# Kernel tuning notes

Hardware: AMD Instinct MI355X
Metric: run time of the kernel (lower is better)

Reference implementation:

```python
import jax, jax.numpy as jnp
import numpy as np

# Static multi-scale spatial shapes (H, W) per level; Len_in = sum(H*W) = 17821.
SPATIAL_SHAPES = [(100, 134), (50, 67), (25, 34), (13, 17)]
NH, NL, NP = 8, 4, 4  # n_heads, n_levels, n_points


def setup_inputs() -> dict:
    key = jax.random.key(0)
    ks = iter(jax.random.split(key, 48))
    N, Lq, Dq, Dkv, Dffn = 4, 900, 256, 384, 1024
    f32 = jnp.float32
    Len_in = sum(h * w for h, w in SPATIAL_SHAPES)

    def nrm(shape, s=0.02):
        return jax.random.normal(next(ks), shape, f32) * s

    inp = dict(
        queries=jax.random.normal(next(ks), (N, Lq, Dq), f32),
        features=jax.random.normal(next(ks), (N, Len_in, Dkv), f32),
        reference_points=jax.random.uniform(next(ks), (N, Lq, NL, 2), f32),
        q_pos=jax.random.normal(next(ks), (N, Lq, Dq), f32) * 0.02,
        kv_spatial_shapes=jnp.array(SPATIAL_SHAPES, jnp.int32),
        level_start_index=jnp.array(
            np.cumsum([0] + [h * w for h, w in SPATIAL_SHAPES[:-1]]), jnp.int32),
        # self-MHA params (torch nn.MultiheadAttention layout)
        in_proj_w=nrm((3 * Dq, Dq)), in_proj_b=jnp.zeros((3 * Dq,), f32),
        mha_out_w=nrm((Dq, Dq)), mha_out_b=jnp.zeros((Dq,), f32),
        # MSDeformAttn params
        value_proj_w=nrm((Dq, Dkv)), value_proj_b=jnp.zeros((Dq,), f32),
        samp_off_w=nrm((NH * NL * NP * 2, Dq), 0.005),
        samp_off_b=nrm((NH * NL * NP * 2,), 0.1),
        attn_w_w=nrm((NH * NL * NP, Dq), 0.01),
        attn_w_b=jnp.zeros((NH * NL * NP,), f32),
        out_proj_w=nrm((Dq, Dq)), out_proj_b=jnp.zeros((Dq,), f32),
        # FFN params
        ffn_w1=nrm((Dffn, Dq)), ffn_b1=jnp.zeros((Dffn,), f32),
        ffn_w2=nrm((Dq, Dffn)), ffn_b2=jnp.zeros((Dq,), f32),
        # LayerNorms
        ln1_g=jnp.ones((Dq,), f32), ln1_b=jnp.zeros((Dq,), f32),
        ln2_g=jnp.ones((Dq,), f32), ln2_b=jnp.zeros((Dq,), f32),
        ln3_g=jnp.ones((Dq,), f32), ln3_b=jnp.zeros((Dq,), f32),
    )
    return inp


def layer_norm(x, g, b, eps=1e-5):
    m = x.mean(-1, keepdims=True)
    v = ((x - m) ** 2).mean(-1, keepdims=True)
    return (x - m) * jax.lax.rsqrt(v + eps) * g + b


def mha(q, k, v, Wqkv, bqkv, Wo, bo, nh):
    N, Lq, D = q.shape
    dh = D // nh
    Wq, Wk, Wv = jnp.split(Wqkv, 3, 0)
    bq, bk, bv = jnp.split(bqkv, 3, 0)
    qh = (q @ Wq.T + bq).reshape(N, Lq, nh, dh)
    kh = (k @ Wk.T + bk).reshape(N, -1, nh, dh)
    vh = (v @ Wv.T + bv).reshape(N, -1, nh, dh)
    scale = jnp.asarray(1.0 / np.sqrt(dh), q.dtype)
    s = jnp.einsum('bqhd,bkhd->bhqk', qh, kh) * scale
    a = jax.nn.softmax(s, -1)
    o = jnp.einsum('bhqk,bkhd->bqhd', a, vh).reshape(N, Lq, D)
    return o @ Wo.T + bo


def grid_sample_bilinear(img, grid):
    # img: (B, H, W, D); grid: (B, Lq, P, 2) in [-1, 1] (x, y)
    # torch F.grid_sample, mode='bilinear', padding_mode='zeros', align_corners=False
    B, H, W, D = img.shape
    gx = ((grid[..., 0] + 1.0) * W - 1.0) * 0.5
    gy = ((grid[..., 1] + 1.0) * H - 1.0) * 0.5
    x0 = jnp.floor(gx); y0 = jnp.floor(gy)
    x1 = x0 + 1.0; y1 = y0 + 1.0
    wx1 = gx - x0; wx0 = 1.0 - wx1
    wy1 = gy - y0; wy0 = 1.0 - wy1
    flat = img.reshape(B, H * W, D)

    def gather(xi, yi):
        valid = (xi >= 0) & (xi <= W - 1) & (yi >= 0) & (yi <= H - 1)
        xc = jnp.clip(xi, 0, W - 1).astype(jnp.int32)
        yc = jnp.clip(yi, 0, H - 1).astype(jnp.int32)
        idx = (yc * W + xc).reshape(B, -1)
        v = jnp.take_along_axis(flat, idx[..., None], axis=1)
        v = v.reshape(B, xi.shape[1], xi.shape[2], D)
        return v * valid[..., None].astype(img.dtype)

    out = (gather(x0, y0) * (wx0 * wy0)[..., None]
           + gather(x1, y0) * (wx1 * wy0)[..., None]
           + gather(x0, y1) * (wx0 * wy1)[..., None]
           + gather(x1, y1) * (wx1 * wy1)[..., None])
    return out


def decoder_layer(queries, features, reference_points, q_pos,
                  in_proj_w, in_proj_b, mha_out_w, mha_out_b,
                  value_proj_w, value_proj_b, samp_off_w, samp_off_b,
                  attn_w_w, attn_w_b, out_proj_w, out_proj_b,
                  ffn_w1, ffn_b1, ffn_w2, ffn_b2,
                  ln1_g, ln1_b, ln2_g, ln2_b, ln3_g, ln3_b):
    N, Lq, D = queries.shape
    dh = D // NH
    # --- self attention (dropout inactive: eval mode) ---
    qk = queries + q_pos
    sa = mha(qk, qk, queries, in_proj_w, in_proj_b, mha_out_w, mha_out_b, NH)
    x = layer_norm(queries + sa, ln1_g, ln1_b)
    # --- multi-scale deformable cross attention ---
    qpe = x + q_pos
    value = (features @ value_proj_w.T + value_proj_b).reshape(N, -1, NH, dh)
    off = (qpe @ samp_off_w.T + samp_off_b).reshape(N, Lq, NH, NL, NP, 2)
    aw = jax.nn.softmax(
        (qpe @ attn_w_w.T + attn_w_b).reshape(N, Lq, NH, NL * NP), -1
    ).reshape(N, Lq, NH, NL, NP)
    # offset normalizer is (W, H) per level
    normalizer = jnp.asarray([[w, h] for h, w in SPATIAL_SHAPES], x.dtype)
    loc = (reference_points[:, :, None, :, None, :]
           + off / normalizer[None, None, None, :, None, :])
    grids = 2.0 * loc - 1.0  # (N, Lq, NH, NL, NP, 2)
    out = jnp.zeros((N, Lq, NH, dh), x.dtype)
    start = 0
    for l, (h, w) in enumerate(SPATIAL_SHAPES):
        v_l = value[:, start:start + h * w]                       # (N, HW, NH, dh)
        v_l = v_l.transpose(0, 2, 1, 3).reshape(N * NH, h, w, dh)
        g_l = grids[:, :, :, l].transpose(0, 2, 1, 3, 4).reshape(N * NH, Lq, NP, 2)
        samp = grid_sample_bilinear(v_l, g_l).reshape(N, NH, Lq, NP, dh)
        w_l = aw[:, :, :, l].transpose(0, 2, 1, 3)                # (N, NH, Lq, NP)
        out = out + jnp.einsum('nhqp,nhqpd->nqhd', w_l, samp)
        start += h * w
    ca = out.reshape(N, Lq, D) @ out_proj_w.T + out_proj_b
    x = layer_norm(x + ca, ln2_g, ln2_b)
    # --- FFN ---
    f = jax.nn.relu(x @ ffn_w1.T + ffn_b1) @ ffn_w2.T + ffn_b2
    return layer_norm(x + f, ln3_g, ln3_b)


def reference(queries, features, reference_points, q_pos,
              kv_spatial_shapes, level_start_index,
              in_proj_w, in_proj_b, mha_out_w, mha_out_b,
              value_proj_w, value_proj_b, samp_off_w, samp_off_b,
              attn_w_w, attn_w_b, out_proj_w, out_proj_b,
              ffn_w1, ffn_b1, ffn_w2, ffn_b2,
              ln1_g, ln1_b, ln2_g, ln2_b, ln3_g, ln3_b):
    # kv_spatial_shapes / level_start_index mirror the torch API; the per-level
    # sizes must be static for jit, so SPATIAL_SHAPES is used internally.
    return decoder_layer(queries, features, reference_points, q_pos,
                         in_proj_w, in_proj_b, mha_out_w, mha_out_b,
                         value_proj_w, value_proj_b, samp_off_w, samp_off_b,
                         attn_w_w, attn_w_b, out_proj_w, out_proj_b,
                         ffn_w1, ffn_b1, ffn_w2, ffn_b2,
                         ln1_g, ln1_b, ln2_g, ln2_b, ln3_g, ln3_b)
```

## Files before the change

kernel.cpp:

```cpp
#include <hip/hip_runtime.h>
#include <cstddef>


typedef unsigned short u16;
typedef short  bf16x8 __attribute__((ext_vector_type(8)));
typedef float  f32x4  __attribute__((ext_vector_type(4)));

constexpr int NB=4, LQ=900, DQ=256, DKV=384, DFFN=1024, NHD=8, DH=32, LEN_IN=17821;
constexpr int MQ     = NB*LQ;
constexpr int MQ_PAD = 3648;
constexpr int MV     = NB*LEN_IN;
constexpr int MV_PAD = 557*128;
constexpr int VT_STRIDE = 912;

#define LN_EPS 1e-5f

__device__ inline u16 f2bf(float f) {
    union { float f; unsigned u; } v; v.f = f;
    unsigned u = v.u;
    u += 0x7fffu + ((u >> 16) & 1u);
    return (u16)(u >> 16);
}
__device__ inline float bf2f(u16 h) {
    union { unsigned u; float f; } v; v.u = ((unsigned)h) << 16; return v.f;
}
__device__ inline void gload_lds16(const u16* g, u16* l) {
    __builtin_amdgcn_global_load_lds(
        (const __attribute__((address_space(1))) unsigned*)g,
        (__attribute__((address_space(3))) unsigned*)l, 16, 0, 0);
}

__global__ void convert_misc_kernel(const float* __restrict__ s0, const float* __restrict__ s1,
        const float* __restrict__ s2, const float* __restrict__ s3, const float* __restrict__ s4,
        const float* __restrict__ s5, const float* __restrict__ s6, const float* __restrict__ s7,
        const float* __restrict__ s8, u16* __restrict__ dst) {
    int i4 = blockIdx.x * 256 + threadIdx.x;
    if (i4 >= 492544) return;
    size_t e = (size_t)i4 * 4;
    const float* src; size_t b;
    if      (e < 196608)  { src = s0; b = 0; }
    else if (e < 262144)  { src = s1; b = 196608; }
    else if (e < 360448)  { src = s2; b = 262144; }
    else if (e < 425984)  { src = s3; b = 360448; }
    else if (e < 458752)  { src = s4; b = 425984; }
    else if (e < 524288)  { src = s5; b = 458752; }
    else if (e < 786432)  { src = s6; b = 524288; }
    else if (e < 1048576) { src = s7; b = 786432; }
    else                  { src = s8; b = 1048576; }
    float4 v = *(const float4*)(src + (e - b));
    dst[e] = f2bf(v.x); dst[e+1] = f2bf(v.y); dst[e+2] = f2bf(v.z); dst[e+3] = f2bf(v.w);
}

__global__ void convert_features_kernel(const float* __restrict__ src, u16* __restrict__ dst) {
    size_t i8 = (size_t)blockIdx.x * 256 + threadIdx.x;
    if (i8 >= (size_t)MV * DKV / 8) return;
    const float4 a = ((const float4*)src)[i8 * 2];
    const float4 b = ((const float4*)src)[i8 * 2 + 1];
    u16 h[8] = {f2bf(a.x), f2bf(a.y), f2bf(a.z), f2bf(a.w),
                f2bf(b.x), f2bf(b.y), f2bf(b.z), f2bf(b.w)};
    *(bf16x8*)(dst + i8 * 8) = *(bf16x8*)h;
}

__global__ void addbf_kernel(const float* __restrict__ a, const float* __restrict__ b,
                             u16* __restrict__ c, int n4) {
    int i = blockIdx.x * 256 + threadIdx.x;
    if (i >= n4) return;
    float4 va = ((const float4*)a)[i];
    float4 vb = ((const float4*)b)[i];
    u16 h[4] = {f2bf(va.x + vb.x), f2bf(va.y + vb.y), f2bf(va.z + vb.z), f2bf(va.w + vb.w)};
    *(uint2*)(c + (size_t)i * 4) = *(uint2*)h;
}

template<int BM, int BN, int WM, int WN, int OMODE, bool RELU>
__global__ __launch_bounds__(256) void gemm_bf16(
        const u16* __restrict__ A, const u16* __restrict__ W,
        const float* __restrict__ bias, void* __restrict__ Cout,
        int M, int N, int K) {
    constexpr int BK = 32;
    __shared__ u16 As[BM * BK];
    __shared__ u16 Bs[BN * BK];
    const int bm = blockIdx.y * BM, bn = blockIdx.x * BN;
    const int tid = threadIdx.x, wid = tid >> 6, lane = tid & 63;
    constexpr int NWC = BN / WN;
    const int wr = wid / NWC, wc = wid % NWC;
    constexpr int MR = WM / 16, NR = WN / 16;
    f32x4 acc[MR][NR];
    #pragma unroll
    for (int i = 0; i < MR; ++i)
        #pragma unroll
        for (int j = 0; j < NR; ++j)
            acc[i][j] = (f32x4){0.f, 0.f, 0.f, 0.f};
    const int r16 = lane & 15;
    const int kb  = (lane >> 4) * 8;

    for (int k0 = 0; k0 < K; k0 += BK) {
        #pragma unroll
        for (int i = 0; i < BM / 64; ++i) {
            const int c = i * 256 + tid;
            gload_lds16(A + (size_t)(bm + (c >> 2)) * K + k0 + (c & 3) * 8, &As[c * 8]);
        }
        #pragma unroll
        for (int i = 0; i < BN / 64; ++i) {
            const int c = i * 256 + tid;
            gload_lds16(W + (size_t)(bn + (c >> 2)) * K + k0 + (c & 3) * 8, &Bs[c * 8]);
        }
        __syncthreads();
        bf16x8 af[MR], bfr[NR];
        #pragma unroll
        for (int i = 0; i < MR; ++i)
            af[i] = *(const bf16x8*)&As[(wr * WM + i * 16 + r16) * BK + kb];
        #pragma unroll
        for (int j = 0; j < NR; ++j)
            bfr[j] = *(const bf16x8*)&Bs[(wc * WN + j * 16 + r16) * BK + kb];
        #pragma unroll
        for (int i = 0; i < MR; ++i)
            #pragma unroll
            for (int j = 0; j < NR; ++j)
                acc[i][j] = __builtin_amdgcn_mfma_f32_16x16x32_bf16(af[i], bfr[j], acc[i][j], 0, 0, 0);
        __syncthreads();
    }
    float* Cf = (float*)Cout;
    u16*   Cb = (u16*)Cout;
    #pragma unroll
    for (int i = 0; i < MR; ++i) {
        #pragma unroll
        for (int j = 0; j < NR; ++j) {
            const int col   = bn + wc * WN + j * 16 + r16;
            const int rbase = bm + wr * WM + i * 16 + (lane >> 4) * 4;
            const float bv = bias[col];
            if (OMODE == 2) {
                if (rbase < M) {
                    const int nb_ = rbase / LQ, tok = rbase - nb_ * LQ;
                    u16 hv[4];
                    #pragma unroll
                    for (int r = 0; r < 4; ++r) hv[r] = f2bf(acc[i][j][r] + bv);
                    uint2 pk; pk.x = hv[0] | ((unsigned)hv[1] << 16);
                    pk.y = hv[2] | ((unsigned)hv[3] << 16);
                    *(uint2*)(Cb + ((size_t)((nb_ * NHD + (col >> 5)) * DH + (col & 31))) * VT_STRIDE + tok) = pk;
                }
            } else {
                #pragma unroll
                for (int r = 0; r < 4; ++r) {
                    const int row = rbase + r;
                    if (row < M) {
                        float v = acc[i][j][r] + bv;
                        if (RELU) v = fmaxf(v, 0.f);
                        if (OMODE == 1) Cb[(size_t)row * N + col] = f2bf(v);
                        else            Cf[(size_t)row * N + col] = v;
                    }
                }
            }
        }
    }
}

__global__ __launch_bounds__(256) void attn_mfma_kernel(
        const u16* __restrict__ qk_proj,
        const u16* __restrict__ vT,
        u16* __restrict__ attno) {
    constexpr int NT = 29;
    const int n = blockIdx.z, h = blockIdx.y;
    const int q0 = blockIdx.x * 64;
    const int tid = threadIdx.x, wid = tid >> 6;
    const int lane = tid & 63;
    const int lq = lane & 15, lg = lane >> 4;

    __shared__ u16 Kb[2][32 * 32];
    __shared__ u16 Vb[2][32 * 32];
    __shared__ u16 Pl[4][16 * 40];

    const int qg  = q0 + wid * 16 + lq;
    const int qcl = min(qg, LQ - 1);
    const bf16x8 qf = *(const bf16x8*)(qk_proj + ((size_t)(n * LQ + qcl)) * 512 + h * 32 + lg * 8);

    f32x4 acc0 = {0.f, 0.f, 0.f, 0.f};
    f32x4 acc1 = {0.f, 0.f, 0.f, 0.f};
    float m = -1e30f, l = 0.f;
    const float scale = 0.17677669529663687f;

    const int ks8 = (lg ^ ((lq >> 1) & 3)) * 8;

#define STAGE(buf, kt)                                                            \
    do {                                                                          \
        if (tid < 128) {                                                          \
            const int key = tid >> 2, sl = tid & 3;                               \
            const int slg = sl ^ ((key >> 1) & 3);                                \
            const int tok = min((kt) * 32 + key, LQ - 1);                         \
            gload_lds16(qk_proj + ((size_t)(n * LQ + tok)) * 512 + 256 + h * 32 + slg * 8, \
                        &Kb[buf][tid * 8]);                                       \
        } else {                                                                  \
            const int t2 = tid - 128;                                             \
            const int dim = t2 >> 2, sl = t2 & 3;                                 \
            const int slg = sl ^ ((dim >> 1) & 3);                                \
            gload_lds16(vT + ((size_t)((n * NHD + h) * DH + dim)) * VT_STRIDE + (kt) * 32 + slg * 8, \
                        &Vb[buf][t2 * 8]);                                        \
        }                                                                         \
    } while (0)

    STAGE(0, 0);
    __syncthreads();

    for (int kt = 0; kt < NT; ++kt) {
        const int cur = kt & 1;
        if (kt + 1 < NT) STAGE(cur ^ 1, kt + 1);

        const u16* Kc = Kb[cur];
        const u16* Vc = Vb[cur];

        const bf16x8 kf0 = *(const bf16x8*)(Kc + lq * 32 + ks8);
        const bf16x8 kf1 = *(const bf16x8*)(Kc + (16 + lq) * 32 + ks8);
        f32x4 c0 = {0.f, 0.f, 0.f, 0.f}, c1 = {0.f, 0.f, 0.f, 0.f};
        c0 = __builtin_amdgcn_mfma_f32_16x16x32_bf16(kf0, qf, c0, 0, 0, 0);
        c1 = __builtin_amdgcn_mfma_f32_16x16x32_bf16(kf1, qf, c1, 0, 0, 0);

        float s[8];
        const int kbase = kt * 32 + lg * 4;
        #pragma unroll
        for (int r = 0; r < 4; ++r) {
            s[r]     = (kbase + r      < LQ) ? c0[r] * scale : -1e30f;
            s[4 + r] = (kbase + 16 + r < LQ) ? c1[r] * scale : -1e30f;
        }
        float tmax = s[0];
        #pragma unroll
        for (int i = 1; i < 8; ++i) tmax = fmaxf(tmax, s[i]);
        tmax = fmaxf(tmax, __shfl_xor(tmax, 16));
        tmax = fmaxf(tmax, __shfl_xor(tmax, 32));
        const float mnew = fmaxf(m, tmax);
        const float corr = __expf(m - mnew);
        l *= corr;
        #pragma unroll
        for (int r = 0; r < 4; ++r) { acc0[r] *= corr; acc1[r] *= corr; }
        float p[8], ps = 0.f;
        #pragma unroll
        for (int i = 0; i < 8; ++i) { p[i] = __expf(s[i] - mnew); ps += p[i]; }
        ps += __shfl_xor(ps, 16);
        ps += __shfl_xor(ps, 32);
        l += ps;
        m = mnew;

        u16* Pw = Pl[wid];
        {
            uint2 w0, w1;
            w0.x = f2bf(p[0]) | ((unsigned)f2bf(p[1]) << 16);
            w0.y = f2bf(p[2]) | ((unsigned)f2bf(p[3]) << 16);
            w1.x = f2bf(p[4]) | ((unsigned)f2bf(p[5]) << 16);
            w1.y = f2bf(p[6]) | ((unsigned)f2bf(p[7]) << 16);
            *(uint2*)(Pw + lq * 40 + lg * 4)      = w0;
            *(uint2*)(Pw + lq * 40 + 16 + lg * 4) = w1;
        }
        asm volatile("s_waitcnt lgkmcnt(0)" ::: "memory");
        __builtin_amdgcn_sched_barrier(0);
        const bf16x8 pt = *(const bf16x8*)(Pw + lq * 40 + lg * 8);

        const bf16x8 vf0 = *(const bf16x8*)(Vc + lq * 32 + ks8);
        const bf16x8 vf1 = *(const bf16x8*)(Vc + (16 + lq) * 32 + ks8);
        acc0 = __builtin_amdgcn_mfma_f32_16x16x32_bf16(vf0, pt, acc0, 0, 0, 0);
        acc1 = __builtin_amdgcn_mfma_f32_16x16x32_bf16(vf1, pt, acc1, 0, 0, 0);

        __syncthreads();
    }
#undef STAGE

    if (qg < LQ) {
        const float inv = 1.f / l;
        u16* op = attno + ((size_t)(n * LQ + qg)) * DQ + h * DH;
        uint2 o0, o1;
        o0.x = f2bf(acc0[0] * inv) | ((unsigned)f2bf(acc0[1] * inv) << 16);
        o0.y = f2bf(acc0[2] * inv) | ((unsigned)f2bf(acc0[3] * inv) << 16);
        o1.x = f2bf(acc1[0] * inv) | ((unsigned)f2bf(acc1[1] * inv) << 16);
        o1.y = f2bf(acc1[2] * inv) | ((unsigned)f2bf(acc1[3] * inv) << 16);
        *(uint2*)(op + lg * 4)      = o0;
        *(uint2*)(op + 16 + lg * 4) = o1;
    }
}

template<bool WBF>
__global__ __launch_bounds__(64) void ln_kernel(
        const float* __restrict__ a, const float* __restrict__ b,
        const float* __restrict__ g, const float* __restrict__ beta,
        float* __restrict__ outf, u16* __restrict__ outb) {
    const int row = blockIdx.x;
    const int lane = threadIdx.x;
    const float* ap = &a[(size_t)row * DQ];
    const float* bp = &b[(size_t)row * DQ];
    float x[4];
    float s = 0.f;
    #pragma unroll
    for (int i = 0; i < 4; ++i) { x[i] = ap[lane + i * 64] + bp[lane + i * 64]; s += x[i]; }
    #pragma unroll
    for (int off = 32; off > 0; off >>= 1) s += __shfl_xor(s, off);
    const float mean = s * (1.f / DQ);
    float v = 0.f;
    #pragma unroll
    for (int i = 0; i < 4; ++i) { const float d = x[i] - mean; v += d * d; }
    #pragma unroll
    for (int off = 32; off > 0; off >>= 1) v += __shfl_xor(v, off);
    const float rstd = rsqrtf(v * (1.f / DQ) + LN_EPS);
    #pragma unroll
    for (int i = 0; i < 4; ++i) {
        const int c = lane + i * 64;
        const float y = (x[i] - mean) * rstd * g[c] + beta[c];
        outf[(size_t)row * DQ + c] = y;
        if (WBF) outb[(size_t)row * DQ + c] = f2bf(y);
    }
}

__global__ void softmax16_kernel(const float* __restrict__ in, float* __restrict__ out, int total) {
    const int i = blockIdx.x * blockDim.x + threadIdx.x;
    if (i >= total) return;
    const float* p = &in[(size_t)i * 16];
    float mx = -1e30f;
    float e[16];
    #pragma unroll
    for (int j = 0; j < 16; ++j) mx = fmaxf(mx, p[j]);
    float sum = 0.f;
    #pragma unroll
    for (int j = 0; j < 16; ++j) { e[j] = __expf(p[j] - mx); sum += e[j]; }
    const float inv = 1.f / sum;
    #pragma unroll
    for (int j = 0; j < 16; ++j) out[(size_t)i * 16 + j] = e[j] * inv;
}

__global__ __launch_bounds__(256) void deform_kernel(
        const u16* __restrict__ value,
        const float* __restrict__ ref_pts,
        const float* __restrict__ off,
        const float* __restrict__ aw,
        u16* __restrict__ out) {
    const int nq = blockIdx.x;
    const int n = nq / LQ, q = nq % LQ;
    const int h = threadIdx.x / DH, d = threadIdx.x % DH;
    const int Hs[4] = {100, 50, 25, 13};
    const int Ws[4] = {134, 67, 34, 17};
    const int LS[4] = {0, 13400, 16750, 17600};
    const float* refp = &ref_pts[((size_t)(n * LQ + q)) * 8];
    const float* offp = &off[((size_t)((n * LQ + q) * NHD + h)) * 32];
    const float* awp  = &aw[((size_t)((n * LQ + q) * NHD + h)) * 16];
    const u16* vb = &value[(size_t)n * LEN_IN * DQ + h * DH + d];
    float acc = 0.f;
    #pragma unroll
    for (int l = 0; l < 4; ++l) {
        const float Wl = (float)Ws[l], Hl = (float)Hs[l];
        const float rx = refp[l * 2 + 0], ry = refp[l * 2 + 1];
        const int Wi = Ws[l], Hi = Hs[l], base = LS[l];
        #pragma unroll
        for (int p = 0; p < 4; ++p) {
            const float ox = offp[(l * 4 + p) * 2 + 0];
            const float oy = offp[(l * 4 + p) * 2 + 1];
            const float gx = (rx + ox / Wl) * Wl - 0.5f;
            const float gy = (ry + oy / Hl) * Hl - 0.5f;
            const float x0f = floorf(gx), y0f = floorf(gy);
            const int x0 = (int)x0f, y0 = (int)y0f;
            const int x1 = x0 + 1, y1 = y0 + 1;
            const float wx1 = gx - x0f, wx0 = 1.f - wx1;
            const float wy1 = gy - y0f, wy0 = 1.f - wy1;
            float sample = 0.f;
            if (x0 >= 0 && x0 < Wi && y0 >= 0 && y0 < Hi)
                sample += wx0 * wy0 * bf2f(vb[(size_t)(base + y0 * Wi + x0) * DQ]);
            if (x1 >= 0 && x1 < Wi && y0 >= 0 && y0 < Hi)
                sample += wx1 * wy0 * bf2f(vb[(size_t)(base + y0 * Wi + x1) * DQ]);
            if (x0 >= 0 && x0 < Wi && y1 >= 0 && y1 < Hi)
                sample += wx0 * wy1 * bf2f(vb[(size_t)(base + y1 * Wi + x0) * DQ]);
            if (x1 >= 0 && x1 < Wi && y1 >= 0 && y1 < Hi)
                sample += wx1 * wy1 * bf2f(vb[(size_t)(base + y1 * Wi + x1) * DQ]);
            acc += awp[l * 4 + p] * sample;
        }
    }
    out[((size_t)(n * LQ + q)) * DQ + h * DH + d] = f2bf(acc);
}

extern "C" void kernel_launch(void* const* d_in, const int* in_sizes, int n_in,
                              void* d_out, int out_size, void* d_ws, size_t ws_size,
                              hipStream_t stream) {
    const float* queries   = (const float*)d_in[0];
    const float* features  = (const float*)d_in[1];
    const float* ref_pts   = (const float*)d_in[2];
    const float* q_pos     = (const float*)d_in[3];
    const float* in_proj_w = (const float*)d_in[6];
    const float* in_proj_b = (const float*)d_in[7];
    const float* mha_out_w = (const float*)d_in[8];
    const float* mha_out_b = (const float*)d_in[9];
    const float* value_proj_w = (const float*)d_in[10];
    const float* value_proj_b = (const float*)d_in[11];
    const float* samp_off_w = (const float*)d_in[12];
    const float* samp_off_b = (const float*)d_in[13];
    const float* attn_w_w  = (const float*)d_in[14];
    const float* attn_w_b  = (const float*)d_in[15];
    const float* out_proj_w = (const float*)d_in[16];
    const float* out_proj_b = (const float*)d_in[17];
    const float* ffn_w1    = (const float*)d_in[18];
    const float* ffn_b1    = (const float*)d_in[19];
    const float* ffn_w2    = (const float*)d_in[20];
    const float* ffn_b2    = (const float*)d_in[21];
    const float* ln1_g     = (const float*)d_in[22];
    const float* ln1_b     = (const float*)d_in[23];
    const float* ln2_g     = (const float*)d_in[24];
    const float* ln2_b     = (const float*)d_in[25];
    const float* ln3_g     = (const float*)d_in[26];
    const float* ln3_b     = (const float*)d_in[27];

    u16* u = (u16*)d_ws;
    u16* wbf      = u; u += 1982464;
    u16* qk_bf    = u; u += (size_t)MQ_PAD * 256;
    u16* qk_proj  = u; u += (size_t)MQ * 512;
    u16* vT       = u; u += (size_t)NB * NHD * DH * VT_STRIDE + 64;
    u16* attno_bf = u; u += (size_t)MQ_PAD * 256;
    u16* qpe_bf   = u; u += (size_t)MQ_PAD * 256;
    u16* x2_bf    = u; u += (size_t)MQ_PAD * 256;
    u16* dout_bf  = u; u += (size_t)MQ_PAD * 256;
    u16* ffnh_bf  = u; u += (size_t)MQ_PAD * 1024;
    u16* features_bf = u; u += (size_t)MV_PAD * DKV;
    u16* value_bf = u; u += (size_t)MV * 256;

    const u16* wIn    = wbf + 0;
    const u16* wMha   = wbf + 196608;
    const u16* wVal   = wbf + 262144;
    const u16* wSamp  = wbf + 360448;
    const u16* wAttnw = wbf + 425984;
    const u16* wOut   = wbf + 458752;
    const u16* wF1    = wbf + 524288;
    const u16* wF2    = wbf + 786432;
    const u16* queries_bf = wbf + 1048576;

    float* f = (float*)u;
    float* x1    = f; f += (size_t)MQ * 256;
    float* sa    = f; float* x2 = sa; f += (size_t)MQ * 256;
    float* offb  = f; float* ca = offb; f += (size_t)MQ * 256;
    float* awlog = f; float* ffnout = awlog; f += 460800;
    float* awbuf = f; f += 460800;

    const int n4 = MQ * 256 / 4;

    hipLaunchKernelGGL(convert_misc_kernel, dim3(1924), dim3(256), 0, stream,
                       in_proj_w, mha_out_w, value_proj_w, samp_off_w, attn_w_w,
                       out_proj_w, ffn_w1, ffn_w2, queries, wbf);
    hipLaunchKernelGGL(addbf_kernel, dim3((n4 + 255) / 256), dim3(256), 0, stream,
                       queries, q_pos, qk_bf, n4);
    hipLaunchKernelGGL((gemm_bf16<64,64,32,32,1,false>), dim3(8, 57), dim3(256), 0, stream,
                       qk_bf, wIn, in_proj_b, (void*)qk_proj, MQ, 512, 256);
    hipLaunchKernelGGL((gemm_bf16<64,64,32,32,2,false>), dim3(4, 57), dim3(256), 0, stream,
                       queries_bf, wIn + 512 * 256, in_proj_b + 512, (void*)vT, MQ, 256, 256);
    hipLaunchKernelGGL(attn_mfma_kernel, dim3(15, NHD, NB), dim3(256), 0, stream,
                       qk_proj, vT, attno_bf);
    hipLaunchKernelGGL((gemm_bf16<64,64,32,32,0,false>), dim3(4, 57), dim3(256), 0, stream,
                       attno_bf, wMha, mha_out_b, (void*)sa, MQ, 256, 256);
    hipLaunchKernelGGL((ln_kernel<false>), dim3(MQ), dim3(64), 0, stream,
                       queries, sa, ln1_g, ln1_b, x1, (u16*)nullptr);
    hipLaunchKernelGGL(addbf_kernel, dim3((n4 + 255) / 256), dim3(256), 0, stream,
                       x1, q_pos, qpe_bf, n4);
    hipLaunchKernelGGL(convert_features_kernel, dim3(13366), dim3(256), 0, stream,
                       features, features_bf);
    hipLaunchKernelGGL((gemm_bf16<128,128,64,64,1,false>), dim3(2, 557), dim3(256), 0, stream,
                       features_bf, wVal, value_proj_b, (void*)value_bf, MV, 256, DKV);
    hipLaunchKernelGGL((gemm_bf16<64,64,32,32,0,false>), dim3(4, 57), dim3(256), 0, stream,
                       qpe_bf, wSamp, samp_off_b, (void*)offb, MQ, 256, 256);
    hipLaunchKernelGGL((gemm_bf16<64,64,32,32,0,false>), dim3(2, 57), dim3(256), 0, stream,
                       qpe_bf, wAttnw, attn_w_b, (void*)awlog, MQ, 128, 256);
    hipLaunchKernelGGL(softmax16_kernel, dim3((MQ * NHD + 255) / 256), dim3(256), 0, stream,
                       awlog, awbuf, MQ * NHD);
    hipLaunchKernelGGL(deform_kernel, dim3(NB * LQ), dim3(256), 0, stream,
                       value_bf, ref_pts, offb, awbuf, dout_bf);
    hipLaunchKernelGGL((gemm_bf16<64,64,32,32,0,false>), dim3(4, 57), dim3(256), 0, stream,
                       dout_bf, wOut, out_proj_b, (void*)ca, MQ, 256, 256);
    hipLaunchKernelGGL((ln_kernel<true>), dim3(MQ), dim3(64), 0, stream,
                       x1, ca, ln2_g, ln2_b, x2, x2_bf);
    hipLaunchKernelGGL((gemm_bf16<64,64,32,32,1,true>), dim3(16, 57), dim3(256), 0, stream,
                       x2_bf, wF1, ffn_b1, (void*)ffnh_bf, MQ, DFFN, 256);
    hipLaunchKernelGGL((gemm_bf16<64,64,32,32,0,false>), dim3(4, 57), dim3(256), 0, stream,
                       ffnh_bf, wF2, ffn_b2, (void*)ffnout, MQ, 256, DFFN);
    hipLaunchKernelGGL((ln_kernel<false>), dim3(MQ), dim3(64), 0, stream,
                       x2, ffnout, ln3_g, ln3_b, (float*)d_out, (u16*)nullptr);
}
```

Baseline: 426.1 us.

## Fuse feature conversion into value GEMM, merge offset/weight GEMMs, inline softmax

Removes the separate fp32-to-bf16 features conversion pass: a new value-projection GEMM reads fp32 features directly and converts them while staging into LDS. The sampling-offset and attention-weight projections become one GEMM with N=384 and a packed bias, since their weights are adjacent in the bf16 buffer. The softmax over the attention weights now runs inside the deform kernel, and the q_pos add is folded into LayerNorm1. This cuts several launches and a large intermediate round trip through memory. The cost is that the new value GEMM issues synchronous fp32 loads without the async LDS path and uses smaller tiles, and the deform kernel recomputes the softmax in every thread.

```diff
diff --git a/kernel.cpp b/kernel.cpp
--- a/kernel.cpp
+++ b/kernel.cpp
@@ -10,7 +10,6 @@
 constexpr int MQ     = NB*LQ;
 constexpr int MQ_PAD = 3648;
 constexpr int MV     = NB*LEN_IN;
-constexpr int MV_PAD = 557*128;
 constexpr int VT_STRIDE = 912;
 
 #define LN_EPS 1e-5f
@@ -33,9 +32,19 @@
 __global__ void convert_misc_kernel(const float* __restrict__ s0, const float* __restrict__ s1,
         const float* __restrict__ s2, const float* __restrict__ s3, const float* __restrict__ s4,
         const float* __restrict__ s5, const float* __restrict__ s6, const float* __restrict__ s7,
-        const float* __restrict__ s8, u16* __restrict__ dst) {
+        const float* __restrict__ s8, u16* __restrict__ dst,
+        const float* __restrict__ sampb, const float* __restrict__ attnb,
+        float* __restrict__ pbias) {
     int i4 = blockIdx.x * 256 + threadIdx.x;
-    if (i4 >= 492544) return;
+    if (i4 >= 492544) {
+        const int e2 = (i4 - 492544) * 4;
+        if (e2 < 384) {
+            float4 v = (e2 < 256) ? *(const float4*)(sampb + e2)
+                                  : *(const float4*)(attnb + (e2 - 256));
+            *(float4*)(pbias + e2) = v;
+        }
+        return;
+    }
     size_t e = (size_t)i4 * 4;
     const float* src; size_t b;
     if      (e < 196608)  { src = s0; b = 0; }
@@ -49,16 +58,6 @@
     else                  { src = s8; b = 1048576; }
     float4 v = *(const float4*)(src + (e - b));
     dst[e] = f2bf(v.x); dst[e+1] = f2bf(v.y); dst[e+2] = f2bf(v.z); dst[e+3] = f2bf(v.w);
-}
-
-__global__ void convert_features_kernel(const float* __restrict__ src, u16* __restrict__ dst) {
-    size_t i8 = (size_t)blockIdx.x * 256 + threadIdx.x;
-    if (i8 >= (size_t)MV * DKV / 8) return;
-    const float4 a = ((const float4*)src)[i8 * 2];
-    const float4 b = ((const float4*)src)[i8 * 2 + 1];
-    u16 h[8] = {f2bf(a.x), f2bf(a.y), f2bf(a.z), f2bf(a.w),
-                f2bf(b.x), f2bf(b.y), f2bf(b.z), f2bf(b.w)};
-    *(bf16x8*)(dst + i8 * 8) = *(bf16x8*)h;
 }
 
 __global__ void addbf_kernel(const float* __restrict__ a, const float* __restrict__ b,
@@ -154,6 +153,71 @@
     }
 }
 
+__global__ __launch_bounds__(256) void gemm_value_kernel(
+        const float* __restrict__ A, const u16* __restrict__ W,
+        const float* __restrict__ bias, u16* __restrict__ C, int M) {
+    constexpr int BK = 32, BM = 64, K = DKV;
+    __shared__ u16 As[BM * BK];
+    __shared__ u16 Bs[256 * BK];
+    const int bm = blockIdx.x * BM;
+    const int tid = threadIdx.x, wid = tid >> 6, lane = tid & 63;
+    const int r16 = lane & 15, kb = (lane >> 4) * 8;
+    f32x4 acc[4][4];
+    #pragma unroll
+    for (int i = 0; i < 4; ++i)
+        #pragma unroll
+        for (int j = 0; j < 4; ++j)
+            acc[i][j] = (f32x4){0.f, 0.f, 0.f, 0.f};
+
+    const int arow = tid >> 2, ac8 = (tid & 3) * 8;
+    for (int k0 = 0; k0 < K; k0 += BK) {
+        #pragma unroll
+        for (int i = 0; i < 4; ++i) {
+            const int c = i * 256 + tid;
+            gload_lds16(W + (size_t)(c >> 2) * K + k0 + (c & 3) * 8, &Bs[c * 8]);
+        }
+        {
+            float tmp[8] = {0.f, 0.f, 0.f, 0.f, 0.f, 0.f, 0.f, 0.f};
+            if (bm + arow < M) {
+                *(float4*)tmp       = *(const float4*)(A + (size_t)(bm + arow) * K + k0 + ac8);
+                *(float4*)(tmp + 4) = *(const float4*)(A + (size_t)(bm + arow) * K + k0 + ac8 + 4);
+            }
+            u16 h8[8];
+            #pragma unroll
+            for (int j = 0; j < 8; ++j) h8[j] = f2bf(tmp[j]);
+            *(bf16x8*)&As[arow * 32 + ac8] = *(bf16x8*)h8;
+        }
+        __syncthreads();
+        bf16x8 af[4], bfr[4];
+        #pragma unroll
+        for (int i = 0; i < 4; ++i)
+            af[i] = *(const bf16x8*)&As[(i * 16 + r16) * 32 + kb];
+        #pragma unroll
+        for (int j = 0; j < 4; ++j)
+            bfr[j] = *(const bf16x8*)&Bs[(wid * 64 + j * 16 + r16) * 32 + kb];
+        #pragma unroll
+        for (int i = 0; i < 4; ++i)
+            #pragma unroll
+            for (int j = 0; j < 4; ++j)
+                acc[i][j] = __builtin_amdgcn_mfma_f32_16x16x32_bf16(af[i], bfr[j], acc[i][j], 0, 0, 0);
+        __syncthreads();
+    }
+    #pragma unroll
+    for (int i = 0; i < 4; ++i) {
+        #pragma unroll
+        for (int j = 0; j < 4; ++j) {
+            const int col   = wid * 64 + j * 16 + r16;
+            const int rbase = bm + i * 16 + (lane >> 4) * 4;
+            const float bv = bias[col];
+            #pragma unroll
+            for (int r = 0; r < 4; ++r) {
+                const int row = rbase + r;
+                if (row < M) C[(size_t)row * 256 + col] = f2bf(acc[i][j][r] + bv);
+            }
+        }
+    }
+}
+
 __global__ __launch_bounds__(256) void attn_mfma_kernel(
         const u16* __restrict__ qk_proj,
         const u16* __restrict__ vT,
@@ -274,11 +338,12 @@
     }
 }
 
-template<bool WBF>
+template<int MODE>
 __global__ __launch_bounds__(64) void ln_kernel(
         const float* __restrict__ a, const float* __restrict__ b,
         const float* __restrict__ g, const float* __restrict__ beta,
-        float* __restrict__ outf, u16* __restrict__ outb) {
+        float* __restrict__ outf, u16* __restrict__ outb,
+        const float* __restrict__ pos) {
     const int row = blockIdx.x;
     const int lane = threadIdx.x;
     const float* ap = &a[(size_t)row * DQ];
@@ -301,31 +366,15 @@
         const int c = lane + i * 64;
         const float y = (x[i] - mean) * rstd * g[c] + beta[c];
         outf[(size_t)row * DQ + c] = y;
-        if (WBF) outb[(size_t)row * DQ + c] = f2bf(y);
-    }
-}
-
-__global__ void softmax16_kernel(const float* __restrict__ in, float* __restrict__ out, int total) {
-    const int i = blockIdx.x * blockDim.x + threadIdx.x;
-    if (i >= total) return;
-    const float* p = &in[(size_t)i * 16];
-    float mx = -1e30f;
-    float e[16];
-    #pragma unroll
-    for (int j = 0; j < 16; ++j) mx = fmaxf(mx, p[j]);
-    float sum = 0.f;
-    #pragma unroll
-    for (int j = 0; j < 16; ++j) { e[j] = __expf(p[j] - mx); sum += e[j]; }
-    const float inv = 1.f / sum;
-    #pragma unroll
-    for (int j = 0; j < 16; ++j) out[(size_t)i * 16 + j] = e[j] * inv;
+        if (MODE == 1) outb[(size_t)row * DQ + c] = f2bf(y);
+        if (MODE == 2) outb[(size_t)row * DQ + c] = f2bf(y + pos[(size_t)row * DQ + c]);
+    }
 }
 
 __global__ __launch_bounds__(256) void deform_kernel(
         const u16* __restrict__ value,
         const float* __restrict__ ref_pts,
-        const float* __restrict__ off,
-        const float* __restrict__ aw,
+        const float* __restrict__ packed,
         u16* __restrict__ out) {
     const int nq = blockIdx.x;
     const int n = nq / LQ, q = nq % LQ;
@@ -334,8 +383,17 @@
     const int Ws[4] = {134, 67, 34, 17};
     const int LS[4] = {0, 13400, 16750, 17600};
     const float* refp = &ref_pts[((size_t)(n * LQ + q)) * 8];
-    const float* offp = &off[((size_t)((n * LQ + q) * NHD + h)) * 32];
-    const float* awp  = &aw[((size_t)((n * LQ + q) * NHD + h)) * 16];
+    const float* rowp = packed + (size_t)nq * 384;
+    const float* offp = rowp + h * 32;
+    const float* lgp  = rowp + 256 + h * 16;
+    float w[16];
+    float mx = lgp[0];
+    #pragma unroll
+    for (int j = 1; j < 16; ++j) mx = fmaxf(mx, lgp[j]);
+    float sum = 0.f;
+    #pragma unroll
+    for (int j = 0; j < 16; ++j) { w[j] = __expf(lgp[j] - mx); sum += w[j]; }
+    const float winv = 1.f / sum;
     const u16* vb = &value[(size_t)n * LEN_IN * DQ + h * DH + d];
     float acc = 0.f;
     #pragma unroll
@@ -363,10 +421,10 @@
                 sample += wx0 * wy1 * bf2f(vb[(size_t)(base + y1 * Wi + x0) * DQ]);
             if (x1 >= 0 && x1 < Wi && y1 >= 0 && y1 < Hi)
                 sample += wx1 * wy1 * bf2f(vb[(size_t)(base + y1 * Wi + x1) * DQ]);
-            acc += awp[l * 4 + p] * sample;
-        }
-    }
-    out[((size_t)(n * LQ + q)) * DQ + h * DH + d] = f2bf(acc);
+            acc += w[l * 4 + p] * winv * sample;
+        }
+    }
+    out[((size_t)nq) * DQ + h * DH + d] = f2bf(acc);
 }
 
 extern "C" void kernel_launch(void* const* d_in, const int* in_sizes, int n_in,
@@ -409,31 +467,30 @@
     u16* x2_bf    = u; u += (size_t)MQ_PAD * 256;
     u16* dout_bf  = u; u += (size_t)MQ_PAD * 256;
     u16* ffnh_bf  = u; u += (size_t)MQ_PAD * 1024;
-    u16* features_bf = u; u += (size_t)MV_PAD * DKV;
     u16* value_bf = u; u += (size_t)MV * 256;
 
     const u16* wIn    = wbf + 0;
     const u16* wMha   = wbf + 196608;
     const u16* wVal   = wbf + 262144;
-    const u16* wSamp  = wbf + 360448;
-    const u16* wAttnw = wbf + 425984;
+    const u16* wSampA = wbf + 360448;
     const u16* wOut   = wbf + 458752;
     const u16* wF1    = wbf + 524288;
     const u16* wF2    = wbf + 786432;
     const u16* queries_bf = wbf + 1048576;
 
     float* f = (float*)u;
-    float* x1    = f; f += (size_t)MQ * 256;
-    float* sa    = f; float* x2 = sa; f += (size_t)MQ * 256;
-    float* offb  = f; float* ca = offb; f += (size_t)MQ * 256;
-    float* awlog = f; float* ffnout = awlog; f += 460800;
-    float* awbuf = f; f += 460800;
+    float* pbias  = f; f += 384;
+    float* x1     = f; f += (size_t)MQ * 256;
+    float* sa     = f; float* x2 = sa; f += (size_t)MQ * 256;
+    float* packed = f; float* ca = packed; f += (size_t)MQ * 384;
+    float* ffnout = f; f += (size_t)MQ * 256;
 
     const int n4 = MQ * 256 / 4;
 
-    hipLaunchKernelGGL(convert_misc_kernel, dim3(1924), dim3(256), 0, stream,
+    hipLaunchKernelGGL(convert_misc_kernel, dim3(1925), dim3(256), 0, stream,
                        in_proj_w, mha_out_w, value_proj_w, samp_off_w, attn_w_w,
-                       out_proj_w, ffn_w1, ffn_w2, queries, wbf);
+                       out_proj_w, ffn_w1, ffn_w2, queries, wbf,
+                       samp_off_b, attn_w_b, pbias);
     hipLaunchKernelGGL(addbf_kernel, dim3((n4 + 255) / 256), dim3(256), 0, stream,
                        queries, q_pos, qk_bf, n4);
     hipLaunchKernelGGL((gemm_bf16<64,64,32,32,1,false>), dim3(8, 57), dim3(256), 0, stream,
@@ -444,30 +501,22 @@
                        qk_proj, vT, attno_bf);
     hipLaunchKernelGGL((gemm_bf16<64,64,32,32,0,false>), dim3(4, 57), dim3(256), 0, stream,
                        attno_bf, wMha, mha_out_b, (void*)sa, MQ, 256, 256);
-    hipLaunchKernelGGL((ln_kernel<false>), dim3(MQ), dim3(64), 0, stream,
-                       queries, sa, ln1_g, ln1_b, x1, (u16*)nullptr);
-    hipLaunchKernelGGL(addbf_kernel, dim3((n4 + 255) / 256), dim3(256), 0, stream,
-                       x1, q_pos, qpe_bf, n4);
-    hipLaunchKernelGGL(convert_features_kernel, dim3(13366), dim3(256), 0, stream,
-                       features, features_bf);
-    hipLaunchKernelGGL((gemm_bf16<128,128,64,64,1,false>), dim3(2, 557), dim3(256), 0, stream,
-                       features_bf, wVal, value_proj_b, (void*)value_bf, MV, 256, DKV);
-    hipLaunchKernelGGL((gemm_bf16<64,64,32,32,0,false>), dim3(4, 57), dim3(256), 0, stream,
-                       qpe_bf, wSamp, samp_off_b, (void*)offb, MQ, 256, 256);
-    hipLaunchKernelGGL((gemm_bf16<64,64,32,32,0,false>), dim3(2, 57), dim3(256), 0, stream,
-                       qpe_bf, wAttnw, attn_w_b, (void*)awlog, MQ, 128, 256);
-    hipLaunchKernelGGL(softmax16_kernel, dim3((MQ * NHD + 255) / 256), dim3(256), 0, stream,
-                       awlog, awbuf, MQ * NHD);
+    hipLaunchKernelGGL((ln_kernel<2>), dim3(MQ), dim3(64), 0, stream,
+                       queries, sa, ln1_g, ln1_b, x1, qpe_bf, q_pos);
+    hipLaunchKernelGGL(gemm_value_kernel, dim3((MV + 63) / 64), dim3(256), 0, stream,
+                       features, wVal, value_proj_b, value_bf, MV);
+    hipLaunchKernelGGL((gemm_bf16<64,64,32,32,0,false>), dim3(6, 57), dim3(256), 0, stream,
+                       qpe_bf, wSampA, pbias, (void*)packed, MQ, 384, 256);
     hipLaunchKernelGGL(deform_kernel, dim3(NB * LQ), dim3(256), 0, stream,
-                       value_bf, ref_pts, offb, awbuf, dout_bf);
+                       value_bf, ref_pts, packed, dout_bf);
     hipLaunchKernelGGL((gemm_bf16<64,64,32,32,0,false>), dim3(4, 57), dim3(256), 0, stream,
                        dout_bf, wOut, out_proj_b, (void*)ca, MQ, 256, 256);
-    hipLaunchKernelGGL((ln_kernel<true>), dim3(MQ), dim3(64), 0, stream,
-                       x1, ca, ln2_g, ln2_b, x2, x2_bf);
+    hipLaunchKernelGGL((ln_kernel<1>), dim3(MQ), dim3(64), 0, stream,
+                       x1, ca, ln2_g, ln2_b, x2, x2_bf, (const float*)nullptr);
     hipLaunchKernelGGL((gemm_bf16<64,64,32,32,1,true>), dim3(16, 57), dim3(256), 0, stream,
                        x2_bf, wF1, ffn_b1, (void*)ffnh_bf, MQ, DFFN, 256);
     hipLaunchKernelGGL((gemm_bf16<64,64,32,32,0,false>), dim3(4, 57), dim3(256), 0, stream,
                        ffnh_bf, wF2, ffn_b2, (void*)ffnout, MQ, 256, DFFN);
-    hipLaunchKernelGGL((ln_kernel<false>), dim3(MQ), dim3(64), 0, stream,
-                       x2, ffnout, ln3_g, ln3_b, (float*)d_out, (u16*)nullptr);
-}
+    hipLaunchKernelGGL((ln_kernel<0>), dim3(MQ), dim3(64), 0, stream,
+                       x2, ffnout, ln3_g, ln3_b, (float*)d_out, (u16*)nullptr, (const float*)nullptr);
+}
```

After: 401.9 us. 1.06x faster.
